# Performance work log

Measured on AMD Instinct MI355X. Metric: run time of the kernel, lower is better.

Reference implementation:

```python
import jax, jax.numpy as jnp
import numpy as np

N = 50000      # num_nodes
E = 640000     # num_edges
IN = 128       # in_dim
OUT = 128      # out_dim
H = 4          # num_heads
DH = OUT // H  # head_dim = 32
R = 5          # num_relations


def setup_inputs() -> dict:
    key = jax.random.key(0)
    k0, k1, k2, k3 = jax.random.split(key, 4)
    x = jax.random.normal(k0, (N, IN), dtype=jnp.float32)
    # stacked per-relation Linear weights/biases (Linear(in_dim, H*DH))
    Ws = jax.random.normal(k1, (R, IN, H * DH), dtype=jnp.float32) * (1.0 / np.sqrt(IN))
    bs = jnp.zeros((R, H * DH), dtype=jnp.float32)
    edge_index = jax.random.randint(k2, (2, E), 0, N)
    edge_types = jax.random.randint(k3, (E,), 0, R)
    return {"x": x, "Ws": Ws, "bs": bs, "edge_index": edge_index, "edge_types": edge_types}


def reference(x, Ws, bs, edge_index, edge_types):
    """Per-relation linear -> gather(src) -> scatter-add(dst) -> mean, then concat.

    Faithful to GraphAttentionLayer.forward with concat=True (att params are
    unused in the original forward; dropout is identity at inference).
    """
    src, dst = edge_index[0], edge_index[1]
    outs = []
    for r in range(R):  # small fixed relation count
        mask = (edge_types == r)
        mf = mask.astype(x.dtype)  # [E]
        x_r = (x @ Ws[r] + bs[r]).reshape(N, H, DH)          # [N,H,DH]
        msgs = x_r[src] * mf[:, None, None]                   # [E,H,DH] masked gather
        agg = jax.ops.segment_sum(msgs, dst, num_segments=N)  # scatter-add
        deg = jnp.clip(jax.ops.segment_sum(mf, dst, num_segments=N), 1.0)  # bincount.clamp(1)
        outs.append(agg / deg[:, None, None])
    out = jnp.concatenate(outs, axis=-1)  # [N, H, DH*R], DH*R=160 != OUT
    out = out.reshape(N, -1)[:, :OUT]     # view + truncate path of original
    return out
```

## Files before the change

### kernel.cpp

```cpp
#include <hip/hip_runtime.h>

#define GN 50000
#define GE 640000
#define CAPR 16
#define NPLACE 625
#define NGEMM 1563
#define NGRP 313

typedef __attribute__((ext_vector_type(8))) short short8;
typedef __attribute__((ext_vector_type(4))) float float4v;

static __device__ __forceinline__ unsigned short f2bf(float f) {
    union { float f; unsigned u; } v; v.f = f;
    unsigned r = v.u + 0x7FFF + ((v.u >> 16) & 1);
    return (unsigned short)(r >> 16);
}
static __device__ __forceinline__ float bf2f(unsigned short h) {
    union { unsigned u; float f; } v; v.u = ((unsigned)h) << 16;
    return v.f;
}

__global__ __launch_bounds__(256) void prep_kernel(const float* __restrict__ Ws,
                                                   unsigned short* __restrict__ Wtg,
                                                   int* __restrict__ cnt) {
    int i = blockIdx.x * 256 + threadIdx.x;
    if (i < GN * 4) cnt[i] = 0;
    if (i < 128 * 128) {
        int n = i >> 7, k = i & 127;
        Wtg[n * 128 + k] = f2bf(Ws[(n >> 5) * 16384 + k * 128 + (n & 31)]);
    }
}

__global__ __launch_bounds__(256) void combo_kernel(const float* __restrict__ x,
                                                    const unsigned short* __restrict__ Wtg,
                                                    const float* __restrict__ bs,
                                                    unsigned short* __restrict__ yb,
                                                    const int* __restrict__ ei,
                                                    const int* __restrict__ et,
                                                    int* __restrict__ cnt,
                                                    unsigned short* __restrict__ elist) {
    const int b = blockIdx.x;
    const int t = threadIdx.x;
    const int grp = b / 7;
    const int role = b % 7;

    if (role < 2) {
        int p = grp * 2 + role;
        if (p >= NPLACE) return;
        int e = p * 1024 + t * 4;
        int4 r4 = *(const int4*)(et + e);
        int4 s4 = *(const int4*)(ei + e);
        int4 d4 = *(const int4*)(ei + GE + e);
        if (r4.x < 4) {
            int pos = atomicAdd(&cnt[(d4.x << 2) + r4.x], 1);
            if (pos < CAPR) elist[(d4.x << 6) + (r4.x << 4) + pos] = (unsigned short)s4.x;
        }
        if (r4.y < 4) {
            int pos = atomicAdd(&cnt[(d4.y << 2) + r4.y], 1);
            if (pos < CAPR) elist[(d4.y << 6) + (r4.y << 4) + pos] = (unsigned short)s4.y;
        }
        if (r4.z < 4) {
            int pos = atomicAdd(&cnt[(d4.z << 2) + r4.z], 1);
            if (pos < CAPR) elist[(d4.z << 6) + (r4.z << 4) + pos] = (unsigned short)s4.z;
        }
        if (r4.w < 4) {
            int pos = atomicAdd(&cnt[(d4.w << 2) + r4.w], 1);
            if (pos < CAPR) elist[(d4.w << 6) + (r4.w << 4) + pos] = (unsigned short)s4.w;
        }
        return;
    }

    const int tile = grp * 5 + (role - 2);
    if (tile >= NGEMM) return;
    const int wv   = t >> 6;
    const int lane = t & 63;
    const int m    = lane & 15;
    const int quad = lane >> 4;
    const int row0 = tile * 32 + (wv & 1) * 16;
    const int col0 = (wv >> 1) * 64;

    short8 afr[4];
    {
        int grow = row0 + m;
        if (grow > GN - 1) grow = GN - 1;
        const float* xr = x + (size_t)grow * 128 + quad * 8;
        #pragma unroll
        for (int s = 0; s < 4; s++) {
            float4 u0 = *(const float4*)(xr + s * 32);
            float4 u1 = *(const float4*)(xr + s * 32 + 4);
            short8 a;
            a[0] = (short)f2bf(u0.x); a[1] = (short)f2bf(u0.y);
            a[2] = (short)f2bf(u0.z); a[3] = (short)f2bf(u0.w);
            a[4] = (short)f2bf(u1.x); a[5] = (short)f2bf(u1.y);
            a[6] = (short)f2bf(u1.z); a[7] = (short)f2bf(u1.w);
            afr[s] = a;
        }
    }

    float4v acc[4] = {{0.f,0.f,0.f,0.f},{0.f,0.f,0.f,0.f},
                      {0.f,0.f,0.f,0.f},{0.f,0.f,0.f,0.f}};
    #pragma unroll
    for (int c = 0; c < 4; c++) {
        const unsigned short* wb = Wtg + (size_t)(col0 + c * 16 + m) * 128 + quad * 8;
        short8 b0 = *(const short8*)(wb);
        short8 b1 = *(const short8*)(wb + 32);
        short8 b2 = *(const short8*)(wb + 64);
        short8 b3 = *(const short8*)(wb + 96);
        acc[c] = __builtin_amdgcn_mfma_f32_16x16x32_bf16(afr[0], b0, acc[c], 0, 0, 0);
        acc[c] = __builtin_amdgcn_mfma_f32_16x16x32_bf16(afr[1], b1, acc[c], 0, 0, 0);
        acc[c] = __builtin_amdgcn_mfma_f32_16x16x32_bf16(afr[2], b2, acc[c], 0, 0, 0);
        acc[c] = __builtin_amdgcn_mfma_f32_16x16x32_bf16(afr[3], b3, acc[c], 0, 0, 0);
    }

    #pragma unroll
    for (int c = 0; c < 4; c++) {
        int n = col0 + c * 16 + m;
        float bias = bs[(n >> 5) * 128 + (n & 31)];
        #pragma unroll
        for (int reg = 0; reg < 4; reg++) {
            int grow = row0 + quad * 4 + reg;
            if (grow < GN)
                yb[(size_t)grow * 128 + n] = f2bf(acc[c][reg] + bias);
        }
    }
}

__global__ __launch_bounds__(256) void accum_kernel(const unsigned short* __restrict__ yb,
                                                    const int* __restrict__ cnt,
                                                    const unsigned short* __restrict__ elist,
                                                    float* __restrict__ out) {
    int node = blockIdx.x * 8 + (threadIdx.x >> 5);
    int lane = threadIdx.x & 31;
    if (node >= GN) return;
    int4 c4 = *(const int4*)(cnt + (node << 2));
    int pw = ((const int*)(elist + (node << 6)))[lane];
    float* o = out + (size_t)node * 128;
    int degs[4] = {c4.x, c4.y, c4.z, c4.w};

    #pragma unroll
    for (int r = 0; r < 4; r++) {
        int cr  = degs[r];
        int deg = cr < CAPR ? cr : CAPR;
        const unsigned short* yb_r = yb + (r << 5) + lane;
        float a = 0.f;
        #pragma unroll
        for (int sb = 0; sb < CAPR; sb += 4) {
            if (sb < deg) {
                int rem = deg - sb;
                int w0 = __shfl(pw, (r << 3) + (sb >> 1), 32);
                float v0 = bf2f(yb_r[(w0 & 0xFFFF) << 7]);
                float v1 = 0.f, v2 = 0.f, v3 = 0.f;
                if (rem > 1) v1 = bf2f(yb_r[((w0 >> 16) & 0xFFFF) << 7]);
                if (rem > 2) {
                    int w1 = __shfl(pw, (r << 3) + (sb >> 1) + 1, 32);
                    v2 = bf2f(yb_r[(w1 & 0xFFFF) << 7]);
                    if (rem > 3) v3 = bf2f(yb_r[((w1 >> 16) & 0xFFFF) << 7]);
                }
                a += (v0 + v1) + (v2 + v3);
            }
        }
        float inv = 1.f / (float)(cr > 1 ? cr : 1);
        o[(r << 5) + lane] = a * inv;
    }
}

extern "C" void kernel_launch(void* const* d_in, const int* in_sizes, int n_in,
                              void* d_out, int out_size, void* d_ws, size_t ws_size,
                              hipStream_t stream) {
    const float* x  = (const float*)d_in[0];
    const float* Ws = (const float*)d_in[1];
    const float* bs = (const float*)d_in[2];
    const int*   ei = (const int*)d_in[3];
    const int*   et = (const int*)d_in[4];

    float* out = (float*)d_out;
    char* ws = (char*)d_ws;
    unsigned short* yb    = (unsigned short*)ws;
    unsigned short* Wtg   = yb + (size_t)GN * 128;
    int* cnt              = (int*)(Wtg + 128 * 128);
    unsigned short* elist = (unsigned short*)(cnt + GN * 4);

    prep_kernel<<<(GN * 4 + 255) / 256, 256, 0, stream>>>(Ws, Wtg, cnt);
    combo_kernel<<<NGRP * 7, 256, 0, stream>>>(x, Wtg, bs, yb, ei, et, cnt, elist);
    accum_kernel<<<(GN + 7) / 8, 256, 0, stream>>>(yb, cnt, elist, out);
}
```

Measured before the change: 136.8 us.

## Replace capped per-node edge lists with atomic scatter-add and separate normalization

Drops the bucketed per-destination edge list (capped at 16 per relation) and its pull-style gather kernel. The output is now zeroed in prep, degrees are counted in the combo kernel, a new kernel scatters each edge's bf16 message into the output with float atomics, and a final kernel divides by degree. This removes the capacity cap and the elist build, at the cost of heavy float atomic traffic on the output (640K edges × 32 lanes), an extra pass over the 25.6MB output, and a nondeterministic summation order.

```diff
diff --git a/kernel.cpp b/kernel.cpp
--- a/kernel.cpp
+++ b/kernel.cpp
@@ -2,10 +2,10 @@
 
 #define GN 50000
 #define GE 640000
-#define CAPR 16
-#define NPLACE 625
 #define NGEMM 1563
 #define NGRP 313
+#define SCB 2048
+#define KEDGE 40
 
 typedef __attribute__((ext_vector_type(8))) short short8;
 typedef __attribute__((ext_vector_type(4))) float float4v;
@@ -22,8 +22,10 @@
 
 __global__ __launch_bounds__(256) void prep_kernel(const float* __restrict__ Ws,
                                                    unsigned short* __restrict__ Wtg,
-                                                   int* __restrict__ cnt) {
+                                                   int* __restrict__ cnt,
+                                                   float* __restrict__ out) {
     int i = blockIdx.x * 256 + threadIdx.x;
+    if (i < GN * 32) ((float4*)out)[i] = make_float4(0.f, 0.f, 0.f, 0.f);
     if (i < GN * 4) cnt[i] = 0;
     if (i < 128 * 128) {
         int n = i >> 7, k = i & 127;
@@ -37,40 +39,32 @@
                                                     unsigned short* __restrict__ yb,
                                                     const int* __restrict__ ei,
                                                     const int* __restrict__ et,
-                                                    int* __restrict__ cnt,
-                                                    unsigned short* __restrict__ elist) {
+                                                    int* __restrict__ cnt) {
     const int b = blockIdx.x;
     const int t = threadIdx.x;
-    const int grp = b / 7;
-    const int role = b % 7;
+    const int grp = b / 6;
+    const int role = b % 6;
 
-    if (role < 2) {
-        int p = grp * 2 + role;
-        if (p >= NPLACE) return;
-        int e = p * 1024 + t * 4;
-        int4 r4 = *(const int4*)(et + e);
-        int4 s4 = *(const int4*)(ei + e);
-        int4 d4 = *(const int4*)(ei + GE + e);
-        if (r4.x < 4) {
-            int pos = atomicAdd(&cnt[(d4.x << 2) + r4.x], 1);
-            if (pos < CAPR) elist[(d4.x << 6) + (r4.x << 4) + pos] = (unsigned short)s4.x;
-        }
-        if (r4.y < 4) {
-            int pos = atomicAdd(&cnt[(d4.y << 2) + r4.y], 1);
-            if (pos < CAPR) elist[(d4.y << 6) + (r4.y << 4) + pos] = (unsigned short)s4.y;
-        }
-        if (r4.z < 4) {
-            int pos = atomicAdd(&cnt[(d4.z << 2) + r4.z], 1);
-            if (pos < CAPR) elist[(d4.z << 6) + (r4.z << 4) + pos] = (unsigned short)s4.z;
-        }
-        if (r4.w < 4) {
-            int pos = atomicAdd(&cnt[(d4.w << 2) + r4.w], 1);
-            if (pos < CAPR) elist[(d4.w << 6) + (r4.w << 4) + pos] = (unsigned short)s4.w;
+    if (role == 0) {
+        int e = grp * 2048 + t * 8;
+        if (e < GE) {
+            int4 ra = *(const int4*)(et + e);
+            int4 rb = *(const int4*)(et + e + 4);
+            int4 da = *(const int4*)(ei + GE + e);
+            int4 db = *(const int4*)(ei + GE + e + 4);
+            if (ra.x < 4) atomicAdd(&cnt[(da.x << 2) + ra.x], 1);
+            if (ra.y < 4) atomicAdd(&cnt[(da.y << 2) + ra.y], 1);
+            if (ra.z < 4) atomicAdd(&cnt[(da.z << 2) + ra.z], 1);
+            if (ra.w < 4) atomicAdd(&cnt[(da.w << 2) + ra.w], 1);
+            if (rb.x < 4) atomicAdd(&cnt[(db.x << 2) + rb.x], 1);
+            if (rb.y < 4) atomicAdd(&cnt[(db.y << 2) + rb.y], 1);
+            if (rb.z < 4) atomicAdd(&cnt[(db.z << 2) + rb.z], 1);
+            if (rb.w < 4) atomicAdd(&cnt[(db.w << 2) + rb.w], 1);
         }
         return;
     }
 
-    const int tile = grp * 5 + (role - 2);
+    const int tile = grp * 5 + (role - 1);
     if (tile >= NGEMM) return;
     const int wv   = t >> 6;
     const int lane = t & 63;
@@ -125,43 +119,47 @@
     }
 }
 
-__global__ __launch_bounds__(256) void accum_kernel(const unsigned short* __restrict__ yb,
-                                                    const int* __restrict__ cnt,
-                                                    const unsigned short* __restrict__ elist,
-                                                    float* __restrict__ out) {
+__global__ __launch_bounds__(256) void scatter_kernel(const unsigned short* __restrict__ yb,
+                                                      const int* __restrict__ ei,
+                                                      const int* __restrict__ et,
+                                                      float* __restrict__ out) {
+    const int g    = blockIdx.x * 8 + (threadIdx.x >> 5);
+    const int lane = threadIdx.x & 31;
+    const int base = g * KEDGE;
+
+    for (int j = 0; j < KEDGE; j += 4) {
+        int e = base + j;
+        if (e >= GE) break;
+        int4 r4 = *(const int4*)(et + e);
+        int4 s4 = *(const int4*)(ei + e);
+        int4 d4 = *(const int4*)(ei + GE + e);
+        int c0 = r4.x < 4 ? r4.x : 3;
+        int c1 = r4.y < 4 ? r4.y : 3;
+        int c2 = r4.z < 4 ? r4.z : 3;
+        int c3 = r4.w < 4 ? r4.w : 3;
+        float v0 = bf2f(yb[(size_t)s4.x * 128 + (c0 << 5) + lane]);
+        float v1 = bf2f(yb[(size_t)s4.y * 128 + (c1 << 5) + lane]);
+        float v2 = bf2f(yb[(size_t)s4.z * 128 + (c2 << 5) + lane]);
+        float v3 = bf2f(yb[(size_t)s4.w * 128 + (c3 << 5) + lane]);
+        if (r4.x < 4) atomicAdd(out + (size_t)d4.x * 128 + (r4.x << 5) + lane, v0);
+        if (r4.y < 4) atomicAdd(out + (size_t)d4.y * 128 + (r4.y << 5) + lane, v1);
+        if (r4.z < 4) atomicAdd(out + (size_t)d4.z * 128 + (r4.z << 5) + lane, v2);
+        if (r4.w < 4) atomicAdd(out + (size_t)d4.w * 128 + (r4.w << 5) + lane, v3);
+    }
+}
+
+__global__ __launch_bounds__(256) void norm_kernel(const int* __restrict__ cnt,
+                                                   float* __restrict__ out) {
     int node = blockIdx.x * 8 + (threadIdx.x >> 5);
     int lane = threadIdx.x & 31;
     if (node >= GN) return;
-    int4 c4 = *(const int4*)(cnt + (node << 2));
-    int pw = ((const int*)(elist + (node << 6)))[lane];
+    int4 c = *(const int4*)(cnt + (node << 2));
     float* o = out + (size_t)node * 128;
-    int degs[4] = {c4.x, c4.y, c4.z, c4.w};
-
-    #pragma unroll
-    for (int r = 0; r < 4; r++) {
-        int cr  = degs[r];
-        int deg = cr < CAPR ? cr : CAPR;
-        const unsigned short* yb_r = yb + (r << 5) + lane;
-        float a = 0.f;
-        #pragma unroll
-        for (int sb = 0; sb < CAPR; sb += 4) {
-            if (sb < deg) {
-                int rem = deg - sb;
-                int w0 = __shfl(pw, (r << 3) + (sb >> 1), 32);
-                float v0 = bf2f(yb_r[(w0 & 0xFFFF) << 7]);
-                float v1 = 0.f, v2 = 0.f, v3 = 0.f;
-                if (rem > 1) v1 = bf2f(yb_r[((w0 >> 16) & 0xFFFF) << 7]);
-                if (rem > 2) {
-                    int w1 = __shfl(pw, (r << 3) + (sb >> 1) + 1, 32);
-                    v2 = bf2f(yb_r[(w1 & 0xFFFF) << 7]);
-                    if (rem > 3) v3 = bf2f(yb_r[((w1 >> 16) & 0xFFFF) << 7]);
-                }
-                a += (v0 + v1) + (v2 + v3);
-            }
-        }
-        float inv = 1.f / (float)(cr > 1 ? cr : 1);
-        o[(r << 5) + lane] = a * inv;
-    }
+    float v0 = o[lane], v1 = o[32 + lane], v2 = o[64 + lane], v3 = o[96 + lane];
+    o[       lane] = v0 / (float)(c.x > 1 ? c.x : 1);
+    o[32   + lane] = v1 / (float)(c.y > 1 ? c.y : 1);
+    o[64   + lane] = v2 / (float)(c.z > 1 ? c.z : 1);
+    o[96   + lane] = v3 / (float)(c.w > 1 ? c.w : 1);
 }
 
 extern "C" void kernel_launch(void* const* d_in, const int* in_sizes, int n_in,
@@ -175,12 +173,12 @@
 
     float* out = (float*)d_out;
     char* ws = (char*)d_ws;
-    unsigned short* yb    = (unsigned short*)ws;
-    unsigned short* Wtg   = yb + (size_t)GN * 128;
-    int* cnt              = (int*)(Wtg + 128 * 128);
-    unsigned short* elist = (unsigned short*)(cnt + GN * 4);
+    unsigned short* yb  = (unsigned short*)ws;
+    unsigned short* Wtg = yb + (size_t)GN * 128;
+    int* cnt            = (int*)(Wtg + 128 * 128);
 
-    prep_kernel<<<(GN * 4 + 255) / 256, 256, 0, stream>>>(Ws, Wtg, cnt);
-    combo_kernel<<<NGRP * 7, 256, 0, stream>>>(x, Wtg, bs, yb, ei, et, cnt, elist);
-    accum_kernel<<<(GN + 7) / 8, 256, 0, stream>>>(yb, cnt, elist, out);
+    prep_kernel<<<6400, 256, 0, stream>>>(Ws, Wtg, cnt, out);
+    combo_kernel<<<NGRP * 6, 256, 0, stream>>>(x, Wtg, bs, yb, ei, et, cnt);
+    scatter_kernel<<<SCB, 256, 0, stream>>>(yb, ei, et, out);
+    norm_kernel<<<(GN + 7) / 8, 256, 0, stream>>>(cnt, out);
 }
```

Result: slower. 180.0 us (+31.6%).
